# Kernel tuning notes

Hardware: AMD Instinct MI355X
Metric: run time of the kernel (lower is better)

## Reference

```python
import jax, jax.numpy as jnp
import numpy as np

B, H, W = 32, 768, 768


def setup_inputs() -> dict:
    key = jax.random.key(0)
    k1, k2 = jax.random.split(key)
    src = jax.random.normal(k1, (B, H, W, 1), dtype=jnp.float32)
    # flow: per-pixel (dx, dy) displacements, a few pixels in magnitude
    flow = jax.random.normal(k2, (B, H, W, 2), dtype=jnp.float32) * 3.0
    return {"src": src, "flow": flow}


def reference(src, flow):
    b, h, w = src.shape[0], src.shape[1], src.shape[2]
    # base sampling grid: grid[..., 0]=x, grid[..., 1]=y (matches tf.meshgrid order)
    xs = jnp.arange(w, dtype=jnp.float32)
    ys = jnp.arange(h, dtype=jnp.float32)
    gx = xs[None, None, :] + flow[..., 0]  # [B,H,W]
    gy = ys[None, :, None] + flow[..., 1]  # [B,H,W]

    x0f = jnp.floor(gx)
    y0f = jnp.floor(gy)
    x1f = x0f + 1.0
    y1f = y0f + 1.0

    # bilinear weights computed from UNCLIPPED corners (as in the original)
    wa = (x1f - gx) * (y1f - gy)
    wb = (gx - x0f) * (y1f - gy)
    wc = (x1f - gx) * (gy - y0f)
    wd = (gx - x0f) * (gy - y0f)

    x0 = jnp.clip(x0f, 0.0, w - 1).astype(jnp.int32)
    x1 = jnp.clip(x1f, 0.0, w - 1).astype(jnp.int32)
    y0 = jnp.clip(y0f, 0.0, h - 1).astype(jnp.int32)
    y1 = jnp.clip(y1f, 0.0, h - 1).astype(jnp.int32)

    # original gathers only channel 0 (last index hard-coded to 0)
    img = src[..., 0]  # [B,H,W]
    bidx = jnp.arange(b)[:, None, None]  # [B,1,1]

    va = img[bidx, y0, x0]
    vb = img[bidx, y0, x1]
    vc = img[bidx, y1, x0]
    vd = img[bidx, y1, x1]

    warped = wa * va + wb * vb + wc * vc + wd * vd  # [B,H,W]
    return warped[..., None]  # [B,H,W,1]
```

## Files before the change

### kernel.cpp

```cpp
#include <hip/hip_runtime.h>


#define BB 32
#define HH 768
#define WW 768
#define HWN (HH * WW)

__global__ __launch_bounds__(256) void st_warp_kernel(
    const float* __restrict__ src,
    const float* __restrict__ flow,
    float* __restrict__ out,
    int n)
{
    int p = blockIdx.x * blockDim.x + threadIdx.x;
    if (p >= n) return;

    int b   = p / HWN;
    int rem = p - b * HWN;
    int y   = rem / WW;
    int x   = rem - y * WW;

    float2 f = reinterpret_cast<const float2*>(flow)[p];
    float gx = (float)x + f.x;
    float gy = (float)y + f.y;

    float x0f = floorf(gx);
    float y0f = floorf(gy);
    float x1f = x0f + 1.0f;
    float y1f = y0f + 1.0f;

    float wxe = gx - x0f;
    float wxw = x1f - gx;
    float wys = gy - y0f;
    float wyn = y1f - gy;
    float wa = wxw * wyn;
    float wb = wxe * wyn;
    float wc = wxw * wys;
    float wd = wxe * wys;

    int x0 = (int)fminf(fmaxf(x0f, 0.0f), (float)(WW - 1));
    int x1 = (int)fminf(fmaxf(x1f, 0.0f), (float)(WW - 1));
    int y0 = (int)fminf(fmaxf(y0f, 0.0f), (float)(HH - 1));
    int y1 = (int)fminf(fmaxf(y1f, 0.0f), (float)(HH - 1));

    const float* img = src + b * HWN;
    int r0 = y0 * WW;
    int r1 = y1 * WW;
    float va = img[r0 + x0];
    float vb = img[r0 + x1];
    float vc = img[r1 + x0];
    float vd = img[r1 + x1];

    out[p] = wa * va + wb * vb + wc * vc + wd * vd;
}

extern "C" void kernel_launch(void* const* d_in, const int* in_sizes, int n_in,
                              void* d_out, int out_size, void* d_ws, size_t ws_size,
                              hipStream_t stream) {
    const float* src  = (const float*)d_in[0];
    const float* flow = (const float*)d_in[1];
    float* out = (float*)d_out;

    int n = BB * HWN;
    int block = 256;
    int grid = (n + block - 1) / block;
    st_warp_kernel<<<grid, block, 0, stream>>>(src, flow, out, n);
}
```

Baseline: 330.8 us.

## Process four pixels per thread in 2D tiles with vector nontemporal I/O

Restructures the warp kernel to a 3D grid of 64x16 pixel tiles per batch image, with each thread handling four horizontally adjacent pixels. Flow is read with two 16-byte nontemporal loads and output written with one 16-byte nontemporal store, and the per-pixel integer divisions for index decomposition are removed. The 2D tiling is meant to improve cache locality of the bilinear gathers across rows. In exchange there are fewer threads in flight, and more registers are used per thread.

```diff
diff --git a/kernel.cpp b/kernel.cpp
--- a/kernel.cpp
+++ b/kernel.cpp
@@ -6,52 +6,63 @@
 #define WW 768
 #define HWN (HH * WW)
 
+typedef float fvec4 __attribute__((ext_vector_type(4)));
+
 __global__ __launch_bounds__(256) void st_warp_kernel(
     const float* __restrict__ src,
     const float* __restrict__ flow,
-    float* __restrict__ out,
-    int n)
+    float* __restrict__ out)
 {
-    int p = blockIdx.x * blockDim.x + threadIdx.x;
-    if (p >= n) return;
+    int tx = threadIdx.x & 15;
+    int ty = threadIdx.x >> 4;
+    int xb = blockIdx.x * 64 + tx * 4;
+    int y  = blockIdx.y * 16 + ty;
+    int b  = blockIdx.z;
 
-    int b   = p / HWN;
-    int rem = p - b * HWN;
-    int y   = rem / WW;
-    int x   = rem - y * WW;
+    int p = (b * HH + y) * WW + xb;
 
-    float2 f = reinterpret_cast<const float2*>(flow)[p];
-    float gx = (float)x + f.x;
-    float gy = (float)y + f.y;
-
-    float x0f = floorf(gx);
-    float y0f = floorf(gy);
-    float x1f = x0f + 1.0f;
-    float y1f = y0f + 1.0f;
-
-    float wxe = gx - x0f;
-    float wxw = x1f - gx;
-    float wys = gy - y0f;
-    float wyn = y1f - gy;
-    float wa = wxw * wyn;
-    float wb = wxe * wyn;
-    float wc = wxw * wys;
-    float wd = wxe * wys;
-
-    int x0 = (int)fminf(fmaxf(x0f, 0.0f), (float)(WW - 1));
-    int x1 = (int)fminf(fmaxf(x1f, 0.0f), (float)(WW - 1));
-    int y0 = (int)fminf(fmaxf(y0f, 0.0f), (float)(HH - 1));
-    int y1 = (int)fminf(fmaxf(y1f, 0.0f), (float)(HH - 1));
+    const fvec4* fp = reinterpret_cast<const fvec4*>(flow + 2 * p);
+    fvec4 f01 = __builtin_nontemporal_load(fp);
+    fvec4 f23 = __builtin_nontemporal_load(fp + 1);
 
     const float* img = src + b * HWN;
-    int r0 = y0 * WW;
-    int r1 = y1 * WW;
-    float va = img[r0 + x0];
-    float vb = img[r0 + x1];
-    float vc = img[r1 + x0];
-    float vd = img[r1 + x1];
 
-    out[p] = wa * va + wb * vb + wc * vc + wd * vd;
+    float fx[4] = {f01.x, f01.z, f23.x, f23.z};
+    float fy[4] = {f01.y, f01.w, f23.y, f23.w};
+    float res[4];
+
+    #pragma unroll
+    for (int i = 0; i < 4; ++i) {
+        float gx = (float)(xb + i) + fx[i];
+        float gy = (float)y + fy[i];
+
+        float x0f = floorf(gx);
+        float y0f = floorf(gy);
+        float x1f = x0f + 1.0f;
+        float y1f = y0f + 1.0f;
+
+        float wa = (x1f - gx) * (y1f - gy);
+        float wb = (gx - x0f) * (y1f - gy);
+        float wc = (x1f - gx) * (gy - y0f);
+        float wd = (gx - x0f) * (gy - y0f);
+
+        int x0 = (int)fminf(fmaxf(x0f, 0.0f), (float)(WW - 1));
+        int x1 = (int)fminf(fmaxf(x1f, 0.0f), (float)(WW - 1));
+        int y0 = (int)fminf(fmaxf(y0f, 0.0f), (float)(HH - 1));
+        int y1 = (int)fminf(fmaxf(y1f, 0.0f), (float)(HH - 1));
+
+        int r0 = y0 * WW;
+        int r1 = y1 * WW;
+        float va = img[r0 + x0];
+        float vb = img[r0 + x1];
+        float vc = img[r1 + x0];
+        float vd = img[r1 + x1];
+
+        res[i] = wa * va + wb * vb + wc * vc + wd * vd;
+    }
+
+    fvec4 o = {res[0], res[1], res[2], res[3]};
+    __builtin_nontemporal_store(o, reinterpret_cast<fvec4*>(out + p));
 }
 
 extern "C" void kernel_launch(void* const* d_in, const int* in_sizes, int n_in,
@@ -61,8 +72,6 @@
     const float* flow = (const float*)d_in[1];
     float* out = (float*)d_out;
 
-    int n = BB * HWN;
-    int block = 256;
-    int grid = (n + block - 1) / block;
-    st_warp_kernel<<<grid, block, 0, stream>>>(src, flow, out, n);
+    dim3 grid(WW / 64, HH / 16, BB);
+    st_warp_kernel<<<grid, 256, 0, stream>>>(src, flow, out);
 }
```

Result: faster. 304.9 us (-7.8%).
